# Kernel optimization log

Hardware: AMD Instinct MI355X
Metric: run time of the kernel (lower is better)

Reference implementation:

```python
import jax, jax.numpy as jnp
import numpy as np

B, DZ, DS, DH = 8192, 1024, 64, 4096

def setup_inputs() -> dict:
    key = jax.random.key(0)
    ks = jax.random.split(key, 8)
    r1 = 1.0 / np.sqrt(DZ)   # W1 init range (last dim dz)
    r2 = 1.0 / np.sqrt(DH)   # W2 init range (last dim dim_hidden)
    rc = 1.0 / np.sqrt(DS)   # C init range
    return {
        "z": jax.random.normal(ks[0], (B, DZ), jnp.float32),
        "s": jax.random.normal(ks[1], (B, DS), jnp.float32),
        "A": jnp.full((DZ,), 0.95, jnp.float32),
        "W1": jax.random.uniform(ks[2], (DH, DZ), jnp.float32, -r1, r1),
        "W2": jax.random.uniform(ks[3], (DZ, DH), jnp.float32, -r2, r2),
        "h1": jax.random.normal(ks[4], (DH,), jnp.float32),
        "h2": jax.random.normal(ks[5], (DZ,), jnp.float32),
        "C": jax.random.uniform(ks[6], (DZ, DS), jnp.float32, -rc, rc),
    }

def reference(z, s, A, W1, W2, h1, h2, C):
    # PLRNN step, W_trial=False, mean_center=False, noise=0:
    # z' = A*z + relu(z @ W1.T + h1) @ W2.T + h2 + s @ C.T
    z_activated = jax.nn.relu(z @ W1.T + h1)          # [B, DH]
    return A * z + z_activated @ W2.T + h2 + s @ C.T  # [B, DZ]
```

## Files before the change

kernel.cpp:

```cpp
#include <hip/hip_runtime.h>

#define BB 8192
#define DZ 1024
#define DS 64
#define DH 4096
#define KEXT (DH + DS)

typedef float floatx4 __attribute__((ext_vector_type(4)));
typedef __bf16 bf16x8 __attribute__((ext_vector_type(8)));
typedef __bf16 bf16x4 __attribute__((ext_vector_type(4)));
typedef __attribute__((address_space(1))) void* as1_void_ptr;
typedef __attribute__((address_space(3))) void* as3_void_ptr;

#define WAIT_VM0   3952
#define WAIT_VM6   3958
#define WAIT_LGKM0 49279

__device__ __forceinline__ void async_copy16(const void* g, void* l) {
    __builtin_amdgcn_global_load_lds((as1_void_ptr)g, (as3_void_ptr)l, 16, 0, 0);
}

__device__ __forceinline__ bf16x4 cvt4(float4 v) {
    bf16x4 o = { (__bf16)v.x, (__bf16)v.y, (__bf16)v.z, (__bf16)v.w };
    return o;
}

__global__ void prep_all(const float* __restrict__ z, const float* __restrict__ W1,
                         const float* __restrict__ W2, const float* __restrict__ C,
                         const float* __restrict__ s,
                         __bf16* __restrict__ zb, __bf16* __restrict__ W1b,
                         __bf16* __restrict__ B2b, __bf16* __restrict__ Hb) {
    const int b = blockIdx.x, t = threadIdx.x;
    if (b < 8192) {
        int i = b * 256 + t;
        *(bf16x4*)(zb + (size_t)i * 4) = cvt4(((const float4*)z)[i]);
    } else if (b < 12288) {
        int i = (b - 8192) * 256 + t;
        *(bf16x4*)(W1b + (size_t)i * 4) = cvt4(((const float4*)W1)[i]);
    } else if (b < 13312) {
        int j = b - 12288;
        const float* wrow = W2 + (size_t)j * DH;
        const float* crow = C + (size_t)j * DS;
        __bf16* orow = B2b + (size_t)j * KEXT;
        for (int c = t; c < 520; c += 256) {
            int h = c * 8;
            const float* src = (h < DH) ? (wrow + h) : (crow + (h - DH));
            *(bf16x4*)(orow + h)     = cvt4(*(const float4*)(src));
            *(bf16x4*)(orow + h + 4) = cvt4(*(const float4*)(src + 4));
        }
    } else {
        int i = (b - 13312) * 256 + t;
        int r = i >> 4, k = (i & 15) * 4;
        float4 v = *(const float4*)(s + (size_t)r * DS + k);
        *(bf16x4*)(Hb + (size_t)r * KEXT + DH + k) = cvt4(v);
    }
}


__global__ __launch_bounds__(512, 4) void gemm1_relu(
    const __bf16* __restrict__ Ag, const __bf16* __restrict__ Bg,
    const float* __restrict__ h1, __bf16* __restrict__ Hb)
{
    constexpr int ldA = DZ, ldB = DZ, KITER = DZ / 64;
    __shared__ __align__(16) __bf16 As[256 * 64];
    __shared__ __align__(16) __bf16 Bs[128 * 64];

    const int tid = threadIdx.x;
    const int wave = tid >> 6, lane = tid & 63;
    const int wm = wave >> 1, wn = wave & 1;
    const int row0 = blockIdx.x * 256;
    const int col0 = blockIdx.y * 128;

    const __bf16* pA = Ag + (size_t)(row0 + (tid >> 2)) * ldA + (tid & 3) * 8;
    const __bf16* pB = Bg + (size_t)(col0 + ((tid >> 2) & 127)) * ldB + (tid & 3) * 8;
    __bf16* lA = As + wave * 512;
    __bf16* lB = Bs + wave * 512;

    const __bf16* Afrag = As + (wm * 64 + (lane & 15)) * 32 + (lane >> 4) * 8;
    const __bf16* Bfrag = Bs + (wn * 64 + (lane & 15)) * 32 + (lane >> 4) * 8;

    floatx4 acc[4][4];
#pragma unroll
    for (int i = 0; i < 4; ++i)
#pragma unroll
        for (int j = 0; j < 4; ++j) acc[i][j] = (floatx4)0.0f;

    for (int kt = 0; kt < KITER; ++kt) {
        const __bf16* ak = pA + kt * 64;
        const __bf16* bk = pB + kt * 64;
        async_copy16(ak,                           lA);
        async_copy16(ak + (size_t)128 * ldA,       lA + 4096);
        async_copy16(ak + 32,                      lA + 8192);
        async_copy16(ak + (size_t)128 * ldA + 32,  lA + 8192 + 4096);
        async_copy16(bk,                           lB);
        async_copy16(bk + 32,                      lB + 4096);
        __builtin_amdgcn_s_waitcnt(0);
        __syncthreads();

#pragma unroll
        for (int ks = 0; ks < 2; ++ks) {
            bf16x8 af[4], bfr[4];
#pragma unroll
            for (int i = 0; i < 4; ++i) af[i] = *(const bf16x8*)(Afrag + ks * 8192 + i * 16 * 32);
#pragma unroll
            for (int j = 0; j < 4; ++j) bfr[j] = *(const bf16x8*)(Bfrag + ks * 4096 + j * 16 * 32);
#pragma unroll
            for (int i = 0; i < 4; ++i)
#pragma unroll
                for (int j = 0; j < 4; ++j)
                    acc[i][j] = __builtin_amdgcn_mfma_f32_16x16x32_bf16(af[i], bfr[j], acc[i][j], 0, 0, 0);
        }
        __syncthreads();
    }

    const int r0 = row0 + wm * 64 + (lane >> 4) * 4;
    const int c0 = col0 + wn * 64 + (lane & 15);
#pragma unroll
    for (int i = 0; i < 4; ++i) {
#pragma unroll
        for (int j = 0; j < 4; ++j) {
            int c = c0 + j * 16;
            float bias = h1[c];
#pragma unroll
            for (int rg = 0; rg < 4; ++rg) {
                int r = r0 + i * 16 + rg;
                float v = acc[i][j][rg] + bias;
                v = v > 0.0f ? v : 0.0f;
                Hb[(size_t)r * KEXT + c] = (__bf16)v;
            }
        }
    }
}

__global__ __launch_bounds__(512, 2) void gemm2_out(
    const __bf16* __restrict__ Ag, const __bf16* __restrict__ Bg,
    const float* __restrict__ Adiag, const float* __restrict__ h2,
    const __bf16* __restrict__ zb, float* __restrict__ out)
{
    constexpr int ldA = KEXT, ldB = KEXT, KITER = KEXT / 64;
    __shared__ __align__(16) __bf16 As[2 * 256 * 64];
    __shared__ __align__(16) __bf16 Bs[2 * 128 * 64];

    const int tid = threadIdx.x;
    const int wave = tid >> 6, lane = tid & 63;
    const int wm = wave >> 1, wn = wave & 1;
    const int row0 = blockIdx.x * 256;
    const int col0 = blockIdx.y * 128;

    const __bf16* pA = Ag + (size_t)(row0 + (tid >> 2)) * ldA + (tid & 3) * 8;
    const __bf16* pB = Bg + (size_t)(col0 + ((tid >> 2) & 127)) * ldB + (tid & 3) * 8;

    const __bf16* Afrag = As + (wm * 64 + (lane & 15)) * 32 + (lane >> 4) * 8;
    const __bf16* Bfrag = Bs + (wn * 64 + (lane & 15)) * 32 + (lane >> 4) * 8;

    floatx4 acc[4][4];
#pragma unroll
    for (int i = 0; i < 4; ++i)
#pragma unroll
        for (int j = 0; j < 4; ++j) acc[i][j] = (floatx4)0.0f;

    auto issue = [&](int kt, int q) {
        const __bf16* ak = pA + kt * 64;
        const __bf16* bk = pB + kt * 64;
        __bf16* lA = As + q * 16384 + wave * 512;
        __bf16* lB = Bs + q * 8192  + wave * 512;
        async_copy16(ak,                           lA);
        async_copy16(ak + (size_t)128 * ldA,       lA + 4096);
        async_copy16(ak + 32,                      lA + 8192);
        async_copy16(ak + (size_t)128 * ldA + 32,  lA + 8192 + 4096);
        async_copy16(bk,                           lB);
        async_copy16(bk + 32,                      lB + 4096);
    };

    issue(0, 0);

    for (int kt = 0; kt < KITER; ++kt) {
        const int p = kt & 1;
        if (kt + 1 < KITER) {
            issue(kt + 1, p ^ 1);
            __builtin_amdgcn_s_waitcnt(WAIT_VM6);
        } else {
            __builtin_amdgcn_s_waitcnt(WAIT_VM0);
        }
        __builtin_amdgcn_s_barrier();

#pragma unroll
        for (int ks = 0; ks < 2; ++ks) {
            const __bf16* Ab = Afrag + p * 16384 + ks * 8192;
            const __bf16* Bb = Bfrag + p * 8192  + ks * 4096;
            bf16x8 af[4], bfr[4];
#pragma unroll
            for (int i = 0; i < 4; ++i) af[i] = *(const bf16x8*)(Ab + i * 16 * 32);
#pragma unroll
            for (int j = 0; j < 4; ++j) bfr[j] = *(const bf16x8*)(Bb + j * 16 * 32);
#pragma unroll
            for (int i = 0; i < 4; ++i)
#pragma unroll
                for (int j = 0; j < 4; ++j)
                    acc[i][j] = __builtin_amdgcn_mfma_f32_16x16x32_bf16(af[i], bfr[j], acc[i][j], 0, 0, 0);
        }

        __builtin_amdgcn_s_waitcnt(WAIT_LGKM0);
        __builtin_amdgcn_s_barrier();
    }

    const int r0 = row0 + wm * 64 + (lane >> 4) * 4;
    const int c0 = col0 + wn * 64 + (lane & 15);
#pragma unroll
    for (int i = 0; i < 4; ++i) {
#pragma unroll
        for (int j = 0; j < 4; ++j) {
            const int c = c0 + j * 16;
            const float aj = Adiag[c];
            const float hj = h2[c];
#pragma unroll
            for (int rg = 0; rg < 4; ++rg) {
                const int r = r0 + i * 16 + rg;
                out[(size_t)r * DZ + c] =
                    acc[i][j][rg] + aj * (float)zb[(size_t)r * DZ + c] + hj;
            }
        }
    }
}


extern "C" void kernel_launch(void* const* d_in, const int* in_sizes, int n_in,
                              void* d_out, int out_size, void* d_ws, size_t ws_size,
                              hipStream_t stream) {
    const float* z  = (const float*)d_in[0];
    const float* s  = (const float*)d_in[1];
    const float* A  = (const float*)d_in[2];
    const float* W1 = (const float*)d_in[3];
    const float* W2 = (const float*)d_in[4];
    const float* h1 = (const float*)d_in[5];
    const float* h2 = (const float*)d_in[6];
    const float* C  = (const float*)d_in[7];
    float* out = (float*)d_out;

    char* ws = (char*)d_ws;
    size_t offHb  = 0;
    size_t offZb  = offHb  + (size_t)BB * KEXT * 2;
    size_t offW1b = offZb  + (size_t)BB * DZ * 2;
    size_t offB2b = offW1b + (size_t)DH * DZ * 2;
    __bf16* Hb  = (__bf16*)(ws + offHb);
    __bf16* zb  = (__bf16*)(ws + offZb);
    __bf16* W1b = (__bf16*)(ws + offW1b);
    __bf16* B2b = (__bf16*)(ws + offB2b);

    prep_all<<<13824, 256, 0, stream>>>(z, W1, W2, C, s, zb, W1b, B2b, Hb);
    gemm1_relu<<<dim3(BB / 256, DH / 128), 512, 0, stream>>>(zb, W1b, h1, Hb);
    gemm2_out<<<dim3(BB / 256, DZ / 128), 512, 0, stream>>>(Hb, B2b, A, h2, zb, out);
}
```

Before: 262.2 us.

## Double-buffer gemm1 with 256x256 tiles and XOR-swizzle LDS in both GEMMs

gemm1 moves from a single-buffered 256x128 tile over 64-wide K steps to a double-buffered 256x256 tile over 32-wide K steps. Each wave now owns a 128x64 subtile, and the next tile is prefetched while MFMAs run on the current one. Both GEMMs apply an XOR swizzle to the LDS column layout, meant to cut bank conflicts on fragment reads. The larger tile raises arithmetic intensity but uses more registers (32 accumulator vectors per lane) and lowers occupancy to 2 blocks per CU.

```diff
diff --git a/kernel.cpp b/kernel.cpp
--- a/kernel.cpp
+++ b/kernel.cpp
@@ -13,6 +13,7 @@
 typedef __attribute__((address_space(3))) void* as3_void_ptr;
 
 #define WAIT_VM0   3952
+#define WAIT_VM4   3956
 #define WAIT_VM6   3958
 #define WAIT_LGKM0 49279
 
@@ -24,6 +25,7 @@
     bf16x4 o = { (__bf16)v.x, (__bf16)v.y, (__bf16)v.z, (__bf16)v.w };
     return o;
 }
+
 
 __global__ void prep_all(const float* __restrict__ z, const float* __restrict__ W1,
                          const float* __restrict__ W2, const float* __restrict__ C,
@@ -56,67 +58,78 @@
     }
 }
 
-
-__global__ __launch_bounds__(512, 4) void gemm1_relu(
+__global__ __launch_bounds__(512, 2) void gemm1_relu(
     const __bf16* __restrict__ Ag, const __bf16* __restrict__ Bg,
     const float* __restrict__ h1, __bf16* __restrict__ Hb)
 {
-    constexpr int ldA = DZ, ldB = DZ, KITER = DZ / 64;
-    __shared__ __align__(16) __bf16 As[256 * 64];
-    __shared__ __align__(16) __bf16 Bs[128 * 64];
+    constexpr int ldA = DZ, ldB = DZ, KITER = DZ / 32;
+    __shared__ __align__(16) __bf16 As[2 * 256 * 32];
+    __shared__ __align__(16) __bf16 Bs[2 * 256 * 32];
 
     const int tid = threadIdx.x;
     const int wave = tid >> 6, lane = tid & 63;
-    const int wm = wave >> 1, wn = wave & 1;
+    const int wm = wave >> 2, wn = wave & 3;
     const int row0 = blockIdx.x * 256;
-    const int col0 = blockIdx.y * 128;
-
-    const __bf16* pA = Ag + (size_t)(row0 + (tid >> 2)) * ldA + (tid & 3) * 8;
-    const __bf16* pB = Bg + (size_t)(col0 + ((tid >> 2) & 127)) * ldB + (tid & 3) * 8;
-    __bf16* lA = As + wave * 512;
-    __bf16* lB = Bs + wave * 512;
-
-    const __bf16* Afrag = As + (wm * 64 + (lane & 15)) * 32 + (lane >> 4) * 8;
-    const __bf16* Bfrag = Bs + (wn * 64 + (lane & 15)) * 32 + (lane >> 4) * 8;
-
-    floatx4 acc[4][4];
-#pragma unroll
-    for (int i = 0; i < 4; ++i)
+    const int col0 = blockIdx.y * 256;
+
+    const int csrc = ((tid & 3) ^ ((tid >> 3) & 3)) * 8;
+    const __bf16* pA = Ag + (size_t)(row0 + (tid >> 2)) * ldA + csrc;
+    const __bf16* pB = Bg + (size_t)(col0 + (tid >> 2)) * ldB + csrc;
+
+    const int cswz = ((lane >> 4) ^ ((lane >> 1) & 3)) * 8;
+    const __bf16* Afrag = As + (wm * 128 + (lane & 15)) * 32 + cswz;
+    const __bf16* Bfrag = Bs + (wn * 64  + (lane & 15)) * 32 + cswz;
+
+    floatx4 acc[8][4];
+#pragma unroll
+    for (int i = 0; i < 8; ++i)
 #pragma unroll
         for (int j = 0; j < 4; ++j) acc[i][j] = (floatx4)0.0f;
 
-    for (int kt = 0; kt < KITER; ++kt) {
-        const __bf16* ak = pA + kt * 64;
-        const __bf16* bk = pB + kt * 64;
+    auto issue = [&](int kt, int q) {
+        const __bf16* ak = pA + kt * 32;
+        const __bf16* bk = pB + kt * 32;
+        __bf16* lA = As + q * 8192 + wave * 512;
+        __bf16* lB = Bs + q * 8192 + wave * 512;
         async_copy16(ak,                           lA);
         async_copy16(ak + (size_t)128 * ldA,       lA + 4096);
-        async_copy16(ak + 32,                      lA + 8192);
-        async_copy16(ak + (size_t)128 * ldA + 32,  lA + 8192 + 4096);
         async_copy16(bk,                           lB);
-        async_copy16(bk + 32,                      lB + 4096);
-        __builtin_amdgcn_s_waitcnt(0);
-        __syncthreads();
-
-#pragma unroll
-        for (int ks = 0; ks < 2; ++ks) {
-            bf16x8 af[4], bfr[4];
-#pragma unroll
-            for (int i = 0; i < 4; ++i) af[i] = *(const bf16x8*)(Afrag + ks * 8192 + i * 16 * 32);
-#pragma unroll
-            for (int j = 0; j < 4; ++j) bfr[j] = *(const bf16x8*)(Bfrag + ks * 4096 + j * 16 * 32);
-#pragma unroll
-            for (int i = 0; i < 4; ++i)
-#pragma unroll
-                for (int j = 0; j < 4; ++j)
-                    acc[i][j] = __builtin_amdgcn_mfma_f32_16x16x32_bf16(af[i], bfr[j], acc[i][j], 0, 0, 0);
-        }
-        __syncthreads();
-    }
-
-    const int r0 = row0 + wm * 64 + (lane >> 4) * 4;
+        async_copy16(bk + (size_t)128 * ldB,       lB + 4096);
+    };
+
+    issue(0, 0);
+
+    for (int kt = 0; kt < KITER; ++kt) {
+        const int p = kt & 1;
+        if (kt + 1 < KITER) {
+            issue(kt + 1, p ^ 1);
+            __builtin_amdgcn_s_waitcnt(WAIT_VM4);
+        } else {
+            __builtin_amdgcn_s_waitcnt(WAIT_VM0);
+        }
+        __builtin_amdgcn_s_barrier();
+
+        const __bf16* Ab = Afrag + p * 8192;
+        const __bf16* Bb = Bfrag + p * 8192;
+        bf16x8 af[8], bfr[4];
+#pragma unroll
+        for (int i = 0; i < 8; ++i) af[i] = *(const bf16x8*)(Ab + i * 16 * 32);
+#pragma unroll
+        for (int j = 0; j < 4; ++j) bfr[j] = *(const bf16x8*)(Bb + j * 16 * 32);
+#pragma unroll
+        for (int i = 0; i < 8; ++i)
+#pragma unroll
+            for (int j = 0; j < 4; ++j)
+                acc[i][j] = __builtin_amdgcn_mfma_f32_16x16x32_bf16(af[i], bfr[j], acc[i][j], 0, 0, 0);
+
+        __builtin_amdgcn_s_waitcnt(WAIT_LGKM0);
+        __builtin_amdgcn_s_barrier();
+    }
+
+    const int r0 = row0 + wm * 128 + (lane >> 4) * 4;
     const int c0 = col0 + wn * 64 + (lane & 15);
 #pragma unroll
-    for (int i = 0; i < 4; ++i) {
+    for (int i = 0; i < 8; ++i) {
 #pragma unroll
         for (int j = 0; j < 4; ++j) {
             int c = c0 + j * 16;
@@ -147,11 +160,13 @@
     const int row0 = blockIdx.x * 256;
     const int col0 = blockIdx.y * 128;
 
-    const __bf16* pA = Ag + (size_t)(row0 + (tid >> 2)) * ldA + (tid & 3) * 8;
-    const __bf16* pB = Bg + (size_t)(col0 + ((tid >> 2) & 127)) * ldB + (tid & 3) * 8;
-
-    const __bf16* Afrag = As + (wm * 64 + (lane & 15)) * 32 + (lane >> 4) * 8;
-    const __bf16* Bfrag = Bs + (wn * 64 + (lane & 15)) * 32 + (lane >> 4) * 8;
+    const int csrc = ((tid & 3) ^ ((tid >> 3) & 3)) * 8;
+    const __bf16* pA = Ag + (size_t)(row0 + (tid >> 2)) * ldA + csrc;
+    const __bf16* pB = Bg + (size_t)(col0 + ((tid >> 2) & 127)) * ldB + csrc;
+
+    const int cswz = ((lane >> 4) ^ ((lane >> 1) & 3)) * 8;
+    const __bf16* Afrag = As + (wm * 64 + (lane & 15)) * 32 + cswz;
+    const __bf16* Bfrag = Bs + (wn * 64 + (lane & 15)) * 32 + cswz;
 
     floatx4 acc[4][4];
 #pragma unroll
@@ -248,6 +263,6 @@
     __bf16* B2b = (__bf16*)(ws + offB2b);
 
     prep_all<<<13824, 256, 0, stream>>>(z, W1, W2, C, s, zb, W1b, B2b, Hb);
-    gemm1_relu<<<dim3(BB / 256, DH / 128), 512, 0, stream>>>(zb, W1b, h1, Hb);
+    gemm1_relu<<<dim3(BB / 256, DH / 256), 512, 0, stream>>>(zb, W1b, h1, Hb);
     gemm2_out<<<dim3(BB / 256, DZ / 128), 512, 0, stream>>>(Hb, B2b, A, h2, zb, out);
 }
```

Result: slower. 275.5 us (+5.1%).
